# Optimization experiments

Measured on AMD Instinct MI355X. Metric: run time of the kernel, lower is better.

The kernel has to match this reference:

```python
import jax, jax.numpy as jnp
import numpy as np

NUM_EXPERTS = 8
TOP_K = 2


def setup_inputs() -> dict:
    key = jax.random.key(0)
    k1, k2, k3, k4, k5 = jax.random.split(key, 5)
    H, F, E = 1024, 4096, NUM_EXPERTS
    s = 0.02
    return {
        "hidden_states": jax.random.normal(k1, (2, 2048, H), jnp.float32),
        "w_router": jax.random.normal(k2, (E, H), jnp.float32) * s,
        "w1": jax.random.normal(k3, (E, F, H), jnp.float32) * s,
        "w2": jax.random.normal(k4, (E, H, F), jnp.float32) * s,
        "w3": jax.random.normal(k5, (E, F, H), jnp.float32) * s,
    }


def reference(hidden_states, w_router, w1, w2, w3):
    B, S, H = hidden_states.shape
    x = hidden_states.reshape(-1, H)  # [T, H]
    T = x.shape[0]
    # router (nn.Linear, no bias): logits = x @ W^T
    router_logits = x @ w_router.T  # [T, E]
    probs = jax.nn.softmax(router_logits.astype(jnp.float32), axis=-1)
    top_w, top_e = jax.lax.top_k(probs, TOP_K)  # [T, K]
    top_w = top_w / jnp.sum(top_w, axis=-1, keepdims=True)
    top_w = top_w.astype(x.dtype)
    # dense per-token gate matrix [T, E]; zero where expert not selected
    gates = jnp.zeros((T, NUM_EXPERTS), x.dtype).at[
        jnp.arange(T)[:, None], top_e
    ].add(top_w)
    out = jnp.zeros_like(x)
    for e in range(NUM_EXPERTS):  # fixed small expert loop
        h = jax.nn.silu(x @ w1[e].T) * (x @ w3[e].T)  # [T, F]
        out = out + gates[:, e:e + 1] * (h @ w2[e].T)
    return out.reshape(B, S, H), router_logits
```

## Files before the change

### kernel.cpp

```cpp
#include <hip/hip_runtime.h>
#include <hip/hip_bf16.h>
#include <stdint.h>

#define T_TOK 4096
#define H_DIM 1024
#define F_DIM 4096
#define NE 8

typedef float    f32x4  __attribute__((ext_vector_type(4)));
typedef __bf16   bf16x8 __attribute__((ext_vector_type(8)));
typedef uint16_t u16x8  __attribute__((ext_vector_type(8)));

#define AS1 __attribute__((address_space(1)))
#define AS3 __attribute__((address_space(3)))

__device__ __forceinline__ uint16_t f2bf(float f) {
  return __builtin_bit_cast(uint16_t, __float2bfloat16(f));
}

__device__ __forceinline__ void gld16(const void* g, void* l) {
  __builtin_amdgcn_global_load_lds((const AS1 void*)g, (AS3 void*)l, 16, 0, 0);
}

__global__ __launch_bounds__(256) void router_k(
    const float* __restrict__ x, const float* __restrict__ wr,
    float* __restrict__ logits, uint16_t* __restrict__ xb,
    int* __restrict__ pairTok, float* __restrict__ pairGate,
    int* __restrict__ cnt)
{
  const int lane = threadIdx.x & 63;
  const int wid  = threadIdx.x >> 6;
  const int t    = blockIdx.x * 4 + wid;

  const float* xp = x + (size_t)t * H_DIM + lane * 16;
  f32x4 xv[4];
#pragma unroll
  for (int i = 0; i < 4; ++i) xv[i] = *(const f32x4*)(xp + 4 * i);

  u16x8 o0, o1;
#pragma unroll
  for (int j = 0; j < 4; ++j) {
    o0[j] = f2bf(xv[0][j]); o0[j + 4] = f2bf(xv[1][j]);
    o1[j] = f2bf(xv[2][j]); o1[j + 4] = f2bf(xv[3][j]);
  }
  uint16_t* xbp = xb + (size_t)t * H_DIM + lane * 16;
  *(u16x8*)xbp       = o0;
  *(u16x8*)(xbp + 8) = o1;

  float s[NE];
#pragma unroll
  for (int e = 0; e < NE; ++e) {
    const float* wp = wr + e * H_DIM + lane * 16;
    float acc = 0.f;
#pragma unroll
    for (int i = 0; i < 4; ++i) {
      f32x4 wv = *(const f32x4*)(wp + 4 * i);
#pragma unroll
      for (int j = 0; j < 4; ++j) acc += xv[i][j] * wv[j];
    }
#pragma unroll
    for (int off = 32; off > 0; off >>= 1) acc += __shfl_xor(acc, off, 64);
    s[e] = acc;
  }

  if (lane == 0) {
#pragma unroll
    for (int e = 0; e < NE; ++e) logits[t * NE + e] = s[e];
    int e1 = 0;
#pragma unroll
    for (int e = 1; e < NE; ++e) if (s[e] > s[e1]) e1 = e;
    int e2 = (e1 == 0) ? 1 : 0;
#pragma unroll
    for (int e = 0; e < NE; ++e)
      if (e != e1 && e != e2 && s[e] > s[e2]) e2 = e;
    const float d  = s[e2] - s[e1];
    const float g1 = 1.f / (1.f + __expf(d));
    const float g2 = 1.f - g1;
    int i1 = atomicAdd(cnt + e1, 1);
    pairTok[e1 * T_TOK + i1] = t;  pairGate[e1 * T_TOK + i1] = g1;
    int i2 = atomicAdd(cnt + e2, 1);
    pairTok[e2 * T_TOK + i2] = t;  pairGate[e2 * T_TOK + i2] = g2;
  }
}

__global__ void prefix_k(const int* __restrict__ cnt, int* __restrict__ base) {
  if (threadIdx.x == 0) {
    int b = 0;
#pragma unroll
    for (int e = 0; e < NE; ++e) { base[e] = b; b += cnt[e]; }
  }
}

__global__ __launch_bounds__(256, 2) void ffn1_k(
    const uint16_t* __restrict__ xb, const float* __restrict__ w1,
    const float* __restrict__ w3, uint16_t* __restrict__ hbuf,
    const int* __restrict__ pairTok, const int* __restrict__ cnt,
    const int* __restrict__ base)
{
  const int e    = blockIdx.z;
  const int cnte = cnt[e];
  const int m0   = blockIdx.y * 128;
  if (m0 >= cnte) return;
  const int n0   = blockIdx.x * 128;
  const int tid  = threadIdx.x;
  const int lane = tid & 63;
  const int wid  = tid >> 6;
  const int wm   = (wid >> 1) * 64;
  const int wn   = (wid & 1) * 64;

  __shared__ __align__(16) uint16_t lsA [128 * 64];
  __shared__ __align__(16) uint16_t lsB1[128 * 64];
  __shared__ __align__(16) uint16_t lsB3[128 * 64];

  const float* w1e = w1 + (size_t)e * F_DIM * H_DIM;
  const float* w3e = w3 + (size_t)e * F_DIM * H_DIM;

  const uint16_t* asrc[4];
  const float*    b1src[4];
  const float*    b3src[4];
#pragma unroll
  for (int q = 0; q < 4; ++q) {
    const int c = q * 256 + tid;
    const int row = c >> 3, pos = c & 7;
    const int kc  = pos ^ (row & 7);
    int ar = m0 + row; if (ar >= cnte) ar = cnte - 1;
    const int tok = pairTok[e * T_TOK + ar];
    asrc[q]  = xb + (size_t)tok * H_DIM + kc * 8;
    b1src[q] = w1e + (size_t)(n0 + row) * H_DIM + kc * 8;
    b3src[q] = w3e + (size_t)(n0 + row) * H_DIM + kc * 8;
  }

  const f32x4 fz = {0.f, 0.f, 0.f, 0.f};
  f32x4 acc1[4][4], acc3[4][4];
#pragma unroll
  for (int i = 0; i < 4; ++i)
#pragma unroll
    for (int j = 0; j < 4; ++j) { acc1[i][j] = fz; acc3[i][j] = fz; }

  for (int kt = 0; kt < H_DIM; kt += 64) {
    __syncthreads();
#pragma unroll
    for (int q = 0; q < 4; ++q) {
      const int c = q * 256 + tid;
      gld16(asrc[q] + kt, &lsA[c * 8]);
    }
#pragma unroll
    for (int q = 0; q < 4; ++q) {
      const int c = q * 256 + tid;
      const float* s1 = b1src[q] + kt;
      const float* s3 = b3src[q] + kt;
      f32x4 a0 = *(const f32x4*)s1;
      f32x4 a1 = *(const f32x4*)(s1 + 4);
      f32x4 c0 = *(const f32x4*)s3;
      f32x4 c1 = *(const f32x4*)(s3 + 4);
      u16x8 ob1, ob3;
#pragma unroll
      for (int j = 0; j < 4; ++j) {
        ob1[j] = f2bf(a0[j]); ob1[j + 4] = f2bf(a1[j]);
        ob3[j] = f2bf(c0[j]); ob3[j + 4] = f2bf(c1[j]);
      }
      *(u16x8*)&lsB1[c * 8] = ob1;
      *(u16x8*)&lsB3[c * 8] = ob3;
    }
    __syncthreads();
#pragma unroll
    for (int ks = 0; ks < 2; ++ks) {
      bf16x8 af[4], b1f[4], b3f[4];
      const int kg = ks * 4 + (lane >> 4);
#pragma unroll
      for (int i = 0; i < 4; ++i) {
        const int ar = wm + i * 16 + (lane & 15);
        af[i]  = *(const bf16x8*)&lsA [ar * 64 + ((kg ^ (ar & 7)) * 8)];
        const int br = wn + i * 16 + (lane & 15);
        b1f[i] = *(const bf16x8*)&lsB1[br * 64 + ((kg ^ (br & 7)) * 8)];
        b3f[i] = *(const bf16x8*)&lsB3[br * 64 + ((kg ^ (br & 7)) * 8)];
      }
#pragma unroll
      for (int i = 0; i < 4; ++i)
#pragma unroll
        for (int j = 0; j < 4; ++j) {
          acc1[i][j] = __builtin_amdgcn_mfma_f32_16x16x32_bf16(af[i], b1f[j], acc1[i][j], 0, 0, 0);
          acc3[i][j] = __builtin_amdgcn_mfma_f32_16x16x32_bf16(af[i], b3f[j], acc3[i][j], 0, 0, 0);
        }
    }
  }

  const int be = base[e];
#pragma unroll
  for (int i = 0; i < 4; ++i) {
#pragma unroll
    for (int r = 0; r < 4; ++r) {
      const int lrow = m0 + wm + i * 16 + (lane >> 4) * 4 + r;
      if (lrow < cnte) {
        uint16_t* hp = hbuf + (size_t)(be + lrow) * F_DIM + n0 + wn + (lane & 15);
#pragma unroll
        for (int j = 0; j < 4; ++j) {
          const float a  = acc1[i][j][r];
          const float hv = (a / (1.f + __expf(-a))) * acc3[i][j][r];
          hp[j * 16] = f2bf(hv);
        }
      }
    }
  }
}

__global__ __launch_bounds__(256, 2) void ffn2_k(
    const uint16_t* __restrict__ hbuf, const float* __restrict__ w2,
    float* __restrict__ out, const int* __restrict__ pairTok,
    const float* __restrict__ pairGate, const int* __restrict__ cnt,
    const int* __restrict__ base)
{
  const int e    = blockIdx.z;
  const int cnte = cnt[e];
  const int m0   = blockIdx.y * 128;
  if (m0 >= cnte) return;
  const int n0   = blockIdx.x * 128;
  const int tid  = threadIdx.x;
  const int lane = tid & 63;
  const int wid  = tid >> 6;
  const int wm   = (wid >> 1) * 64;
  const int wn   = (wid & 1) * 64;

  __shared__ __align__(16) uint16_t lsA[128 * 64];
  __shared__ __align__(16) uint16_t lsB[128 * 64];

  const int be = base[e];
  const float* w2e = w2 + (size_t)e * H_DIM * F_DIM;

  const uint16_t* asrc[4];
  const float*    bsrc[4];
#pragma unroll
  for (int q = 0; q < 4; ++q) {
    const int c = q * 256 + tid;
    const int row = c >> 3, pos = c & 7;
    const int kc  = pos ^ (row & 7);
    int rr = m0 + row; if (rr >= cnte) rr = cnte - 1;
    asrc[q] = hbuf + (size_t)(be + rr) * F_DIM + kc * 8;
    bsrc[q] = w2e + (size_t)(n0 + row) * F_DIM + kc * 8;
  }

  const f32x4 fz = {0.f, 0.f, 0.f, 0.f};
  f32x4 acc[4][4];
#pragma unroll
  for (int i = 0; i < 4; ++i)
#pragma unroll
    for (int j = 0; j < 4; ++j) acc[i][j] = fz;

  for (int kt = 0; kt < F_DIM; kt += 64) {
    __syncthreads();
#pragma unroll
    for (int q = 0; q < 4; ++q) {
      const int c = q * 256 + tid;
      gld16(asrc[q] + kt, &lsA[c * 8]);
    }
#pragma unroll
    for (int q = 0; q < 4; ++q) {
      const int c = q * 256 + tid;
      const float* sb = bsrc[q] + kt;
      f32x4 b0 = *(const f32x4*)sb;
      f32x4 b1 = *(const f32x4*)(sb + 4);
      u16x8 ob;
#pragma unroll
      for (int j = 0; j < 4; ++j) { ob[j] = f2bf(b0[j]); ob[j + 4] = f2bf(b1[j]); }
      *(u16x8*)&lsB[c * 8] = ob;
    }
    __syncthreads();
#pragma unroll
    for (int ks = 0; ks < 2; ++ks) {
      bf16x8 af[4], bf[4];
      const int kg = ks * 4 + (lane >> 4);
#pragma unroll
      for (int i = 0; i < 4; ++i) {
        const int ar = wm + i * 16 + (lane & 15);
        af[i] = *(const bf16x8*)&lsA[ar * 64 + ((kg ^ (ar & 7)) * 8)];
        const int br = wn + i * 16 + (lane & 15);
        bf[i] = *(const bf16x8*)&lsB[br * 64 + ((kg ^ (br & 7)) * 8)];
      }
#pragma unroll
      for (int i = 0; i < 4; ++i)
#pragma unroll
        for (int j = 0; j < 4; ++j)
          acc[i][j] = __builtin_amdgcn_mfma_f32_16x16x32_bf16(af[i], bf[j], acc[i][j], 0, 0, 0);
    }
  }

#pragma unroll
  for (int i = 0; i < 4; ++i) {
#pragma unroll
    for (int r = 0; r < 4; ++r) {
      const int lrow = m0 + wm + i * 16 + (lane >> 4) * 4 + r;
      if (lrow < cnte) {
        const int   t = pairTok [e * T_TOK + lrow];
        const float g = pairGate[e * T_TOK + lrow];
        float* op = out + (size_t)t * H_DIM + n0 + wn + (lane & 15);
#pragma unroll
        for (int j = 0; j < 4; ++j)
          unsafeAtomicAdd(op + j * 16, g * acc[i][j][r]);
      }
    }
  }
}

extern "C" void kernel_launch(void* const* d_in, const int* in_sizes, int n_in,
                              void* d_out, int out_size, void* d_ws, size_t ws_size,
                              hipStream_t stream)
{
  const float* x  = (const float*)d_in[0];
  const float* wr = (const float*)d_in[1];
  const float* w1 = (const float*)d_in[2];
  const float* w2 = (const float*)d_in[3];
  const float* w3 = (const float*)d_in[4];
  float* out    = (float*)d_out;
  float* logits = out + (size_t)T_TOK * H_DIM;

  uint8_t* ws = (uint8_t*)d_ws;
  const size_t XB_OFF   = 0;
  const size_t HB_OFF   = XB_OFF + (size_t)T_TOK * H_DIM * 2;
  const size_t PT_OFF   = HB_OFF + (size_t)2 * T_TOK * F_DIM * 2;
  const size_t PG_OFF   = PT_OFF + (size_t)NE * T_TOK * 4;
  const size_t CNT_OFF  = PG_OFF + (size_t)NE * T_TOK * 4;
  const size_t BASE_OFF = CNT_OFF + 64;
  const size_t NEED     = BASE_OFF + 64;
  if (ws_size < NEED) return;

  uint16_t* xb      = (uint16_t*)(ws + XB_OFF);
  uint16_t* hb      = (uint16_t*)(ws + HB_OFF);
  int*      pairTok = (int*)(ws + PT_OFF);
  float*    pairGate= (float*)(ws + PG_OFF);
  int*      cnt     = (int*)(ws + CNT_OFF);
  int*      basep   = (int*)(ws + BASE_OFF);

  hipMemsetAsync(out, 0, (size_t)T_TOK * H_DIM * sizeof(float), stream);
  hipMemsetAsync(cnt, 0, 64, stream);
  router_k<<<T_TOK / 4, 256, 0, stream>>>(x, wr, logits, xb, pairTok, pairGate, cnt);
  prefix_k<<<1, 64, 0, stream>>>(cnt, basep);
  ffn1_k<<<dim3(F_DIM / 128, T_TOK / 128, NE), 256, 0, stream>>>(xb, w1, w3, hb, pairTok, cnt, basep);
  ffn2_k<<<dim3(H_DIM / 128, T_TOK / 128, NE), 256, 0, stream>>>(hb, w2, out, pairTok, pairGate, cnt, basep);
}
```

Measured before the change: 569.9 us.

## Pre-convert expert weights to bf16 and stream them via direct LDS loads

Adds a conversion kernel that turns w1, w3 and w2 into bf16 copies in workspace on every call. New FFN kernels then load both activations and weights with global_load_lds into XOR-swizzled LDS tiles, replacing the fp32 weight loads with in-kernel conversion. The extra pass reads about 400MB of fp32 weights and writes 200MB of bf16, in exchange for simpler, cheaper GEMM inner loops. This path runs only if the workspace holds the three bf16 weight copies; otherwise the old kernels are used.

Result: slower. 742.4 us (+30.3%).

```diff
diff --git a/kernel.cpp b/kernel.cpp
--- a/kernel.cpp
+++ b/kernel.cpp
@@ -20,6 +20,20 @@
 
 __device__ __forceinline__ void gld16(const void* g, void* l) {
   __builtin_amdgcn_global_load_lds((const AS1 void*)g, (AS3 void*)l, 16, 0, 0);
+}
+
+__global__ __launch_bounds__(256) void cvt_k(const float* __restrict__ src,
+                                             uint16_t* __restrict__ dst, int n8) {
+  const int stride = gridDim.x * blockDim.x;
+  for (int i = blockIdx.x * blockDim.x + threadIdx.x; i < n8; i += stride) {
+    const float* s = src + (size_t)i * 8;
+    f32x4 a = *(const f32x4*)s;
+    f32x4 b = *(const f32x4*)(s + 4);
+    u16x8 o;
+#pragma unroll
+    for (int j = 0; j < 4; ++j) { o[j] = f2bf(a[j]); o[j + 4] = f2bf(b[j]); }
+    *(u16x8*)(dst + (size_t)i * 8) = o;
+  }
 }
 
 __global__ __launch_bounds__(256) void router_k(
@@ -90,6 +104,192 @@
     for (int e = 0; e < NE; ++e) { base[e] = b; b += cnt[e]; }
   }
 }
+
+
+__global__ __launch_bounds__(256, 3) void ffn1b_k(
+    const uint16_t* __restrict__ xb, const uint16_t* __restrict__ w1b,
+    const uint16_t* __restrict__ w3b, uint16_t* __restrict__ hbuf,
+    const int* __restrict__ pairTok, const int* __restrict__ cnt,
+    const int* __restrict__ base)
+{
+  const int e    = blockIdx.z;
+  const int cnte = cnt[e];
+  const int m0   = blockIdx.y * 128;
+  if (m0 >= cnte) return;
+  const int n0   = blockIdx.x * 128;
+  const int tid  = threadIdx.x;
+  const int lane = tid & 63;
+  const int wid  = tid >> 6;
+  const int wm   = (wid >> 1) * 64;
+  const int wn   = (wid & 1) * 64;
+
+  __shared__ __align__(16) uint16_t lsA [128 * 64];
+  __shared__ __align__(16) uint16_t lsB1[128 * 64];
+  __shared__ __align__(16) uint16_t lsB3[128 * 64];
+
+  const uint16_t* w1e = w1b + (size_t)e * F_DIM * H_DIM;
+  const uint16_t* w3e = w3b + (size_t)e * F_DIM * H_DIM;
+
+  const uint16_t* asrc[4];
+  const uint16_t* b1src[4];
+  const uint16_t* b3src[4];
+#pragma unroll
+  for (int q = 0; q < 4; ++q) {
+    const int c = q * 256 + tid;
+    const int row = c >> 3, pos = c & 7;
+    const int kc  = pos ^ (row & 7);
+    int ar = m0 + row; if (ar >= cnte) ar = cnte - 1;
+    const int tok = pairTok[e * T_TOK + ar];
+    asrc[q]  = xb  + (size_t)tok * H_DIM + kc * 8;
+    b1src[q] = w1e + (size_t)(n0 + row) * H_DIM + kc * 8;
+    b3src[q] = w3e + (size_t)(n0 + row) * H_DIM + kc * 8;
+  }
+
+  const f32x4 fz = {0.f, 0.f, 0.f, 0.f};
+  f32x4 acc1[4][4], acc3[4][4];
+#pragma unroll
+  for (int i = 0; i < 4; ++i)
+#pragma unroll
+    for (int j = 0; j < 4; ++j) { acc1[i][j] = fz; acc3[i][j] = fz; }
+
+  for (int kt = 0; kt < H_DIM; kt += 64) {
+    __syncthreads();
+#pragma unroll
+    for (int q = 0; q < 4; ++q) {
+      const int c = q * 256 + tid;
+      gld16(asrc[q]  + kt, &lsA [c * 8]);
+      gld16(b1src[q] + kt, &lsB1[c * 8]);
+      gld16(b3src[q] + kt, &lsB3[c * 8]);
+    }
+    __syncthreads();
+#pragma unroll
+    for (int ks = 0; ks < 2; ++ks) {
+      bf16x8 af[4], b1f[4], b3f[4];
+      const int kg = ks * 4 + (lane >> 4);
+#pragma unroll
+      for (int i = 0; i < 4; ++i) {
+        const int ar = wm + i * 16 + (lane & 15);
+        af[i]  = *(const bf16x8*)&lsA [ar * 64 + ((kg ^ (ar & 7)) * 8)];
+        const int br = wn + i * 16 + (lane & 15);
+        b1f[i] = *(const bf16x8*)&lsB1[br * 64 + ((kg ^ (br & 7)) * 8)];
+        b3f[i] = *(const bf16x8*)&lsB3[br * 64 + ((kg ^ (br & 7)) * 8)];
+      }
+#pragma unroll
+      for (int i = 0; i < 4; ++i)
+#pragma unroll
+        for (int j = 0; j < 4; ++j) {
+          acc1[i][j] = __builtin_amdgcn_mfma_f32_16x16x32_bf16(af[i], b1f[j], acc1[i][j], 0, 0, 0);
+          acc3[i][j] = __builtin_amdgcn_mfma_f32_16x16x32_bf16(af[i], b3f[j], acc3[i][j], 0, 0, 0);
+        }
+    }
+  }
+
+  const int be = base[e];
+#pragma unroll
+  for (int i = 0; i < 4; ++i) {
+#pragma unroll
+    for (int r = 0; r < 4; ++r) {
+      const int lrow = m0 + wm + i * 16 + (lane >> 4) * 4 + r;
+      if (lrow < cnte) {
+        uint16_t* hp = hbuf + (size_t)(be + lrow) * F_DIM + n0 + wn + (lane & 15);
+#pragma unroll
+        for (int j = 0; j < 4; ++j) {
+          const float a  = acc1[i][j][r];
+          const float hv = (a / (1.f + __expf(-a))) * acc3[i][j][r];
+          hp[j * 16] = f2bf(hv);
+        }
+      }
+    }
+  }
+}
+
+__global__ __launch_bounds__(256, 3) void ffn2b_k(
+    const uint16_t* __restrict__ hbuf, const uint16_t* __restrict__ w2b,
+    float* __restrict__ out, const int* __restrict__ pairTok,
+    const float* __restrict__ pairGate, const int* __restrict__ cnt,
+    const int* __restrict__ base)
+{
+  const int e    = blockIdx.z;
+  const int cnte = cnt[e];
+  const int m0   = blockIdx.y * 128;
+  if (m0 >= cnte) return;
+  const int n0   = blockIdx.x * 128;
+  const int tid  = threadIdx.x;
+  const int lane = tid & 63;
+  const int wid  = tid >> 6;
+  const int wm   = (wid >> 1) * 64;
+  const int wn   = (wid & 1) * 64;
+
+  __shared__ __align__(16) uint16_t lsA[128 * 64];
+  __shared__ __align__(16) uint16_t lsB[128 * 64];
+
+  const int be = base[e];
+  const uint16_t* w2e = w2b + (size_t)e * H_DIM * F_DIM;
+
+  const uint16_t* asrc[4];
+  const uint16_t* bsrc[4];
+#pragma unroll
+  for (int q = 0; q < 4; ++q) {
+    const int c = q * 256 + tid;
+    const int row = c >> 3, pos = c & 7;
+    const int kc  = pos ^ (row & 7);
+    int rr = m0 + row; if (rr >= cnte) rr = cnte - 1;
+    asrc[q] = hbuf + (size_t)(be + rr) * F_DIM + kc * 8;
+    bsrc[q] = w2e + (size_t)(n0 + row) * F_DIM + kc * 8;
+  }
+
+  const f32x4 fz = {0.f, 0.f, 0.f, 0.f};
+  f32x4 acc[4][4];
+#pragma unroll
+  for (int i = 0; i < 4; ++i)
+#pragma unroll
+    for (int j = 0; j < 4; ++j) acc[i][j] = fz;
+
+  for (int kt = 0; kt < F_DIM; kt += 64) {
+    __syncthreads();
+#pragma unroll
+    for (int q = 0; q < 4; ++q) {
+      const int c = q * 256 + tid;
+      gld16(asrc[q] + kt, &lsA[c * 8]);
+      gld16(bsrc[q] + kt, &lsB[c * 8]);
+    }
+    __syncthreads();
+#pragma unroll
+    for (int ks = 0; ks < 2; ++ks) {
+      bf16x8 af[4], bf[4];
+      const int kg = ks * 4 + (lane >> 4);
+#pragma unroll
+      for (int i = 0; i < 4; ++i) {
+        const int ar = wm + i * 16 + (lane & 15);
+        af[i] = *(const bf16x8*)&lsA[ar * 64 + ((kg ^ (ar & 7)) * 8)];
+        const int br = wn + i * 16 + (lane & 15);
+        bf[i] = *(const bf16x8*)&lsB[br * 64 + ((kg ^ (br & 7)) * 8)];
+      }
+#pragma unroll
+      for (int i = 0; i < 4; ++i)
+#pragma unroll
+        for (int j = 0; j < 4; ++j)
+          acc[i][j] = __builtin_amdgcn_mfma_f32_16x16x32_bf16(af[i], bf[j], acc[i][j], 0, 0, 0);
+    }
+  }
+
+#pragma unroll
+  for (int i = 0; i < 4; ++i) {
+#pragma unroll
+    for (int r = 0; r < 4; ++r) {
+      const int lrow = m0 + wm + i * 16 + (lane >> 4) * 4 + r;
+      if (lrow < cnte) {
+        const int   t = pairTok [e * T_TOK + lrow];
+        const float g = pairGate[e * T_TOK + lrow];
+        float* op = out + (size_t)t * H_DIM + n0 + wn + (lane & 15);
+#pragma unroll
+        for (int j = 0; j < 4; ++j)
+          unsafeAtomicAdd(op + j * 16, g * acc[i][j][r]);
+      }
+    }
+  }
+}
+
 
 __global__ __launch_bounds__(256, 2) void ffn1_k(
     const uint16_t* __restrict__ xb, const float* __restrict__ w1,
@@ -314,14 +514,19 @@
   float* logits = out + (size_t)T_TOK * H_DIM;
 
   uint8_t* ws = (uint8_t*)d_ws;
+  const size_t WELEMS   = (size_t)NE * F_DIM * H_DIM;
   const size_t XB_OFF   = 0;
   const size_t HB_OFF   = XB_OFF + (size_t)T_TOK * H_DIM * 2;
   const size_t PT_OFF   = HB_OFF + (size_t)2 * T_TOK * F_DIM * 2;
   const size_t PG_OFF   = PT_OFF + (size_t)NE * T_TOK * 4;
   const size_t CNT_OFF  = PG_OFF + (size_t)NE * T_TOK * 4;
   const size_t BASE_OFF = CNT_OFF + 64;
-  const size_t NEED     = BASE_OFF + 64;
-  if (ws_size < NEED) return;
+  const size_t W1B_OFF  = BASE_OFF + 64;
+  const size_t W3B_OFF  = W1B_OFF + WELEMS * 2;
+  const size_t W2B_OFF  = W3B_OFF + WELEMS * 2;
+  const size_t NEED_BIG = W2B_OFF + WELEMS * 2;
+  const size_t NEED_SM  = W1B_OFF;
+  if (ws_size < NEED_SM) return;
 
   uint16_t* xb      = (uint16_t*)(ws + XB_OFF);
   uint16_t* hb      = (uint16_t*)(ws + HB_OFF);
@@ -334,6 +539,19 @@
   hipMemsetAsync(cnt, 0, 64, stream);
   router_k<<<T_TOK / 4, 256, 0, stream>>>(x, wr, logits, xb, pairTok, pairGate, cnt);
   prefix_k<<<1, 64, 0, stream>>>(cnt, basep);
-  ffn1_k<<<dim3(F_DIM / 128, T_TOK / 128, NE), 256, 0, stream>>>(xb, w1, w3, hb, pairTok, cnt, basep);
-  ffn2_k<<<dim3(H_DIM / 128, T_TOK / 128, NE), 256, 0, stream>>>(hb, w2, out, pairTok, pairGate, cnt, basep);
-}
+
+  if (ws_size >= NEED_BIG) {
+    uint16_t* w1b = (uint16_t*)(ws + W1B_OFF);
+    uint16_t* w3b = (uint16_t*)(ws + W3B_OFF);
+    uint16_t* w2b = (uint16_t*)(ws + W2B_OFF);
+    const int n8 = (int)(WELEMS / 8);
+    cvt_k<<<2048, 256, 0, stream>>>(w1, w1b, n8);
+    cvt_k<<<2048, 256, 0, stream>>>(w3, w3b, n8);
+    cvt_k<<<2048, 256, 0, stream>>>(w2, w2b, n8);
+    ffn1b_k<<<dim3(F_DIM / 128, T_TOK / 128, NE), 256, 0, stream>>>(xb, w1b, w3b, hb, pairTok, cnt, basep);
+    ffn2b_k<<<dim3(H_DIM / 128, T_TOK / 128, NE), 256, 0, stream>>>(hb, w2b, out, pairTok, pairGate, cnt, basep);
+  } else {
+    ffn1_k<<<dim3(F_DIM / 128, T_TOK / 128, NE), 256, 0, stream>>>(xb, w1, w3, hb, pairTok, cnt, basep);
+    ffn2_k<<<dim3(H_DIM / 128, T_TOK / 128, NE), 256, 0, stream>>>(hb, w2, out, pairTok, pairGate, cnt, basep);
+  }
+}
```

## Double-buffer LDS tiles with register prefetch in both FFN GEMM kernels

Applied to the files above, without the earlier changes.

Both expert GEMM kernels now use two LDS stages with a K-tile of 32 instead of one stage of 64. The next tile's global loads (direct-to-LDS for activations, register loads for fp32 weights) are issued before the MFMA work on the current tile, and the converted weights are stored afterwards, so only one barrier is needed per iteration. This is meant to hide global-load latency behind compute. The trade-off is twice as many loop iterations with shallower MFMA work per barrier, plus extra registers for the prefetched values; ffn2 also raises its launch-bounds occupancy hint from 2 to 3.

Result: slower. 685.5 us (+20.3%).

```diff
diff --git a/kernel.cpp b/kernel.cpp
--- a/kernel.cpp
+++ b/kernel.cpp
@@ -108,24 +108,26 @@
   const int wm   = (wid >> 1) * 64;
   const int wn   = (wid & 1) * 64;
 
-  __shared__ __align__(16) uint16_t lsA [128 * 64];
-  __shared__ __align__(16) uint16_t lsB1[128 * 64];
-  __shared__ __align__(16) uint16_t lsB3[128 * 64];
+  __shared__ __align__(16) uint16_t lsA [2][128 * 32];
+  __shared__ __align__(16) uint16_t lsB1[2][128 * 32];
+  __shared__ __align__(16) uint16_t lsB3[2][128 * 32];
 
   const float* w1e = w1 + (size_t)e * F_DIM * H_DIM;
   const float* w3e = w3 + (size_t)e * F_DIM * H_DIM;
 
-  const uint16_t* asrc[4];
-  const float*    b1src[4];
-  const float*    b3src[4];
-#pragma unroll
-  for (int q = 0; q < 4; ++q) {
+  const uint16_t* asrc[2];
+  const float*    b1src[2];
+  const float*    b3src[2];
+  int cdst[2];
+#pragma unroll
+  for (int q = 0; q < 2; ++q) {
     const int c = q * 256 + tid;
-    const int row = c >> 3, pos = c & 7;
-    const int kc  = pos ^ (row & 7);
+    const int row = c >> 2, pos = c & 3;
+    const int kc  = pos ^ (row & 3);
+    cdst[q] = c * 8;
     int ar = m0 + row; if (ar >= cnte) ar = cnte - 1;
     const int tok = pairTok[e * T_TOK + ar];
-    asrc[q]  = xb + (size_t)tok * H_DIM + kc * 8;
+    asrc[q]  = xb  + (size_t)tok * H_DIM + kc * 8;
     b1src[q] = w1e + (size_t)(n0 + row) * H_DIM + kc * 8;
     b3src[q] = w3e + (size_t)(n0 + row) * H_DIM + kc * 8;
   }
@@ -137,43 +139,57 @@
 #pragma unroll
     for (int j = 0; j < 4; ++j) { acc1[i][j] = fz; acc3[i][j] = fz; }
 
-  for (int kt = 0; kt < H_DIM; kt += 64) {
-    __syncthreads();
-#pragma unroll
-    for (int q = 0; q < 4; ++q) {
-      const int c = q * 256 + tid;
-      gld16(asrc[q] + kt, &lsA[c * 8]);
-    }
-#pragma unroll
-    for (int q = 0; q < 4; ++q) {
-      const int c = q * 256 + tid;
-      const float* s1 = b1src[q] + kt;
-      const float* s3 = b3src[q] + kt;
-      f32x4 a0 = *(const f32x4*)s1;
-      f32x4 a1 = *(const f32x4*)(s1 + 4);
-      f32x4 c0 = *(const f32x4*)s3;
-      f32x4 c1 = *(const f32x4*)(s3 + 4);
+  {
+#pragma unroll
+    for (int q = 0; q < 2; ++q) gld16(asrc[q], &lsA[0][cdst[q]]);
+#pragma unroll
+    for (int q = 0; q < 2; ++q) {
+      f32x4 a0 = *(const f32x4*)b1src[q];
+      f32x4 a1 = *(const f32x4*)(b1src[q] + 4);
+      f32x4 c0 = *(const f32x4*)b3src[q];
+      f32x4 c1 = *(const f32x4*)(b3src[q] + 4);
       u16x8 ob1, ob3;
 #pragma unroll
       for (int j = 0; j < 4; ++j) {
         ob1[j] = f2bf(a0[j]); ob1[j + 4] = f2bf(a1[j]);
         ob3[j] = f2bf(c0[j]); ob3[j + 4] = f2bf(c1[j]);
       }
-      *(u16x8*)&lsB1[c * 8] = ob1;
-      *(u16x8*)&lsB3[c * 8] = ob3;
-    }
-    __syncthreads();
-#pragma unroll
-    for (int ks = 0; ks < 2; ++ks) {
+      *(u16x8*)&lsB1[0][cdst[q]] = ob1;
+      *(u16x8*)&lsB3[0][cdst[q]] = ob3;
+    }
+  }
+  __syncthreads();
+
+  const int NT = H_DIM / 32;
+  for (int t = 0; t < NT; ++t) {
+    const int cur = t & 1;
+    const int nxt = cur ^ 1;
+    const int koff = (t + 1) * 32;
+    const bool pre = (t + 1 < NT);
+
+    f32x4 b1v[2][2], b3v[2][2];
+    if (pre) {
+#pragma unroll
+      for (int q = 0; q < 2; ++q) gld16(asrc[q] + koff, &lsA[nxt][cdst[q]]);
+#pragma unroll
+      for (int q = 0; q < 2; ++q) {
+        b1v[q][0] = *(const f32x4*)(b1src[q] + koff);
+        b1v[q][1] = *(const f32x4*)(b1src[q] + koff + 4);
+        b3v[q][0] = *(const f32x4*)(b3src[q] + koff);
+        b3v[q][1] = *(const f32x4*)(b3src[q] + koff + 4);
+      }
+    }
+
+    {
       bf16x8 af[4], b1f[4], b3f[4];
-      const int kg = ks * 4 + (lane >> 4);
+      const int kg = lane >> 4;
 #pragma unroll
       for (int i = 0; i < 4; ++i) {
         const int ar = wm + i * 16 + (lane & 15);
-        af[i]  = *(const bf16x8*)&lsA [ar * 64 + ((kg ^ (ar & 7)) * 8)];
+        af[i]  = *(const bf16x8*)&lsA [cur][ar * 32 + ((kg ^ (ar & 3)) * 8)];
         const int br = wn + i * 16 + (lane & 15);
-        b1f[i] = *(const bf16x8*)&lsB1[br * 64 + ((kg ^ (br & 7)) * 8)];
-        b3f[i] = *(const bf16x8*)&lsB3[br * 64 + ((kg ^ (br & 7)) * 8)];
+        b1f[i] = *(const bf16x8*)&lsB1[cur][br * 32 + ((kg ^ (br & 3)) * 8)];
+        b3f[i] = *(const bf16x8*)&lsB3[cur][br * 32 + ((kg ^ (br & 3)) * 8)];
       }
 #pragma unroll
       for (int i = 0; i < 4; ++i)
@@ -183,6 +199,21 @@
           acc3[i][j] = __builtin_amdgcn_mfma_f32_16x16x32_bf16(af[i], b3f[j], acc3[i][j], 0, 0, 0);
         }
     }
+
+    if (pre) {
+#pragma unroll
+      for (int q = 0; q < 2; ++q) {
+        u16x8 ob1, ob3;
+#pragma unroll
+        for (int j = 0; j < 4; ++j) {
+          ob1[j] = f2bf(b1v[q][0][j]); ob1[j + 4] = f2bf(b1v[q][1][j]);
+          ob3[j] = f2bf(b3v[q][0][j]); ob3[j + 4] = f2bf(b3v[q][1][j]);
+        }
+        *(u16x8*)&lsB1[nxt][cdst[q]] = ob1;
+        *(u16x8*)&lsB3[nxt][cdst[q]] = ob3;
+      }
+    }
+    __syncthreads();
   }
 
   const int be = base[e];
@@ -204,7 +235,7 @@
   }
 }
 
-__global__ __launch_bounds__(256, 2) void ffn2_k(
+__global__ __launch_bounds__(256, 3) void ffn2_k(
     const uint16_t* __restrict__ hbuf, const float* __restrict__ w2,
     float* __restrict__ out, const int* __restrict__ pairTok,
     const float* __restrict__ pairGate, const int* __restrict__ cnt,
@@ -221,19 +252,21 @@
   const int wm   = (wid >> 1) * 64;
   const int wn   = (wid & 1) * 64;
 
-  __shared__ __align__(16) uint16_t lsA[128 * 64];
-  __shared__ __align__(16) uint16_t lsB[128 * 64];
+  __shared__ __align__(16) uint16_t lsA[2][128 * 32];
+  __shared__ __align__(16) uint16_t lsB[2][128 * 32];
 
   const int be = base[e];
   const float* w2e = w2 + (size_t)e * H_DIM * F_DIM;
 
-  const uint16_t* asrc[4];
-  const float*    bsrc[4];
-#pragma unroll
-  for (int q = 0; q < 4; ++q) {
+  const uint16_t* asrc[2];
+  const float*    bsrc[2];
+  int cdst[2];
+#pragma unroll
+  for (int q = 0; q < 2; ++q) {
     const int c = q * 256 + tid;
-    const int row = c >> 3, pos = c & 7;
-    const int kc  = pos ^ (row & 7);
+    const int row = c >> 2, pos = c & 3;
+    const int kc  = pos ^ (row & 3);
+    cdst[q] = c * 8;
     int rr = m0 + row; if (rr >= cnte) rr = cnte - 1;
     asrc[q] = hbuf + (size_t)(be + rr) * F_DIM + kc * 8;
     bsrc[q] = w2e + (size_t)(n0 + row) * F_DIM + kc * 8;
@@ -246,35 +279,48 @@
 #pragma unroll
     for (int j = 0; j < 4; ++j) acc[i][j] = fz;
 
-  for (int kt = 0; kt < F_DIM; kt += 64) {
-    __syncthreads();
-#pragma unroll
-    for (int q = 0; q < 4; ++q) {
-      const int c = q * 256 + tid;
-      gld16(asrc[q] + kt, &lsA[c * 8]);
-    }
-#pragma unroll
-    for (int q = 0; q < 4; ++q) {
-      const int c = q * 256 + tid;
-      const float* sb = bsrc[q] + kt;
-      f32x4 b0 = *(const f32x4*)sb;
-      f32x4 b1 = *(const f32x4*)(sb + 4);
+  {
+#pragma unroll
+    for (int q = 0; q < 2; ++q) gld16(asrc[q], &lsA[0][cdst[q]]);
+#pragma unroll
+    for (int q = 0; q < 2; ++q) {
+      f32x4 b0 = *(const f32x4*)bsrc[q];
+      f32x4 b1 = *(const f32x4*)(bsrc[q] + 4);
       u16x8 ob;
 #pragma unroll
       for (int j = 0; j < 4; ++j) { ob[j] = f2bf(b0[j]); ob[j + 4] = f2bf(b1[j]); }
-      *(u16x8*)&lsB[c * 8] = ob;
-    }
-    __syncthreads();
-#pragma unroll
-    for (int ks = 0; ks < 2; ++ks) {
+      *(u16x8*)&lsB[0][cdst[q]] = ob;
+    }
+  }
+  __syncthreads();
+
+  const int NT = F_DIM / 32;
+  for (int t = 0; t < NT; ++t) {
+    const int cur = t & 1;
+    const int nxt = cur ^ 1;
+    const int koff = (t + 1) * 32;
+    const bool pre = (t + 1 < NT);
+
+    f32x4 bv[2][2];
+    if (pre) {
+#pragma unroll
+      for (int q = 0; q < 2; ++q) gld16(asrc[q] + koff, &lsA[nxt][cdst[q]]);
+#pragma unroll
+      for (int q = 0; q < 2; ++q) {
+        bv[q][0] = *(const f32x4*)(bsrc[q] + koff);
+        bv[q][1] = *(const f32x4*)(bsrc[q] + koff + 4);
+      }
+    }
+
+    {
       bf16x8 af[4], bf[4];
-      const int kg = ks * 4 + (lane >> 4);
+      const int kg = lane >> 4;
 #pragma unroll
       for (int i = 0; i < 4; ++i) {
         const int ar = wm + i * 16 + (lane & 15);
-        af[i] = *(const bf16x8*)&lsA[ar * 64 + ((kg ^ (ar & 7)) * 8)];
+        af[i] = *(const bf16x8*)&lsA[cur][ar * 32 + ((kg ^ (ar & 3)) * 8)];
         const int br = wn + i * 16 + (lane & 15);
-        bf[i] = *(const bf16x8*)&lsB[br * 64 + ((kg ^ (br & 7)) * 8)];
+        bf[i] = *(const bf16x8*)&lsB[cur][br * 32 + ((kg ^ (br & 3)) * 8)];
       }
 #pragma unroll
       for (int i = 0; i < 4; ++i)
@@ -282,6 +328,17 @@
         for (int j = 0; j < 4; ++j)
           acc[i][j] = __builtin_amdgcn_mfma_f32_16x16x32_bf16(af[i], bf[j], acc[i][j], 0, 0, 0);
     }
+
+    if (pre) {
+#pragma unroll
+      for (int q = 0; q < 2; ++q) {
+        u16x8 ob;
+#pragma unroll
+        for (int j = 0; j < 4; ++j) { ob[j] = f2bf(bv[q][0][j]); ob[j + 4] = f2bf(bv[q][1][j]); }
+        *(u16x8*)&lsB[nxt][cdst[q]] = ob;
+      }
+    }
+    __syncthreads();
   }
 
 #pragma unroll
```

## Replace LDS-tiled ffn1 with register-direct MFMA loads and double buffering

Applied to the files above, without the earlier changes.

Rewrites the gate/up projection kernel to skip shared memory and barriers, loading A and B fragments straight from global memory into registers. Tiles become 256 tokens by 32 columns, and loads are software-pipelined with two register sets. This removes LDS traffic and sync overhead. In exchange, the gathered activation rows are re-read far more often across the many narrow column blocks, and weight reads are less coalesced.

Result: slower. 1.081 ms (+89.8%).

```diff
diff --git a/kernel.cpp b/kernel.cpp
--- a/kernel.cpp
+++ b/kernel.cpp
@@ -99,106 +99,91 @@
 {
   const int e    = blockIdx.z;
   const int cnte = cnt[e];
-  const int m0   = blockIdx.y * 128;
+  const int m0   = blockIdx.y * 256;
   if (m0 >= cnte) return;
-  const int n0   = blockIdx.x * 128;
-  const int tid  = threadIdx.x;
-  const int lane = tid & 63;
-  const int wid  = tid >> 6;
-  const int wm   = (wid >> 1) * 64;
-  const int wn   = (wid & 1) * 64;
-
-  __shared__ __align__(16) uint16_t lsA [128 * 64];
-  __shared__ __align__(16) uint16_t lsB1[128 * 64];
-  __shared__ __align__(16) uint16_t lsB3[128 * 64];
-
-  const float* w1e = w1 + (size_t)e * F_DIM * H_DIM;
-  const float* w3e = w3 + (size_t)e * F_DIM * H_DIM;
-
-  const uint16_t* asrc[4];
-  const float*    b1src[4];
-  const float*    b3src[4];
-#pragma unroll
-  for (int q = 0; q < 4; ++q) {
-    const int c = q * 256 + tid;
-    const int row = c >> 3, pos = c & 7;
-    const int kc  = pos ^ (row & 7);
-    int ar = m0 + row; if (ar >= cnte) ar = cnte - 1;
+  const int n0   = blockIdx.x * 32;
+  const int lane = threadIdx.x & 63;
+  const int wid  = threadIdx.x >> 6;
+  const int wm   = (wid >> 1) * 128;
+  const int wn   = (wid & 1) * 16;
+  const int kg8  = (lane >> 4) * 8;
+
+  const uint16_t* aptr[8];
+#pragma unroll
+  for (int i = 0; i < 8; ++i) {
+    int ar = m0 + wm + i * 16 + (lane & 15);
+    if (ar >= cnte) ar = cnte - 1;
     const int tok = pairTok[e * T_TOK + ar];
-    asrc[q]  = xb + (size_t)tok * H_DIM + kc * 8;
-    b1src[q] = w1e + (size_t)(n0 + row) * H_DIM + kc * 8;
-    b3src[q] = w3e + (size_t)(n0 + row) * H_DIM + kc * 8;
-  }
+    aptr[i] = xb + (size_t)tok * H_DIM + kg8;
+  }
+  const int   nrow = n0 + wn + (lane & 15);
+  const float* b1p = w1 + (size_t)e * F_DIM * H_DIM + (size_t)nrow * H_DIM + kg8;
+  const float* b3p = w3 + (size_t)e * F_DIM * H_DIM + (size_t)nrow * H_DIM + kg8;
 
   const f32x4 fz = {0.f, 0.f, 0.f, 0.f};
-  f32x4 acc1[4][4], acc3[4][4];
-#pragma unroll
-  for (int i = 0; i < 4; ++i)
-#pragma unroll
-    for (int j = 0; j < 4; ++j) { acc1[i][j] = fz; acc3[i][j] = fz; }
-
-  for (int kt = 0; kt < H_DIM; kt += 64) {
-    __syncthreads();
-#pragma unroll
-    for (int q = 0; q < 4; ++q) {
-      const int c = q * 256 + tid;
-      gld16(asrc[q] + kt, &lsA[c * 8]);
-    }
-#pragma unroll
-    for (int q = 0; q < 4; ++q) {
-      const int c = q * 256 + tid;
-      const float* s1 = b1src[q] + kt;
-      const float* s3 = b3src[q] + kt;
-      f32x4 a0 = *(const f32x4*)s1;
-      f32x4 a1 = *(const f32x4*)(s1 + 4);
-      f32x4 c0 = *(const f32x4*)s3;
-      f32x4 c1 = *(const f32x4*)(s3 + 4);
-      u16x8 ob1, ob3;
-#pragma unroll
-      for (int j = 0; j < 4; ++j) {
-        ob1[j] = f2bf(a0[j]); ob1[j + 4] = f2bf(a1[j]);
-        ob3[j] = f2bf(c0[j]); ob3[j + 4] = f2bf(c1[j]);
-      }
-      *(u16x8*)&lsB1[c * 8] = ob1;
-      *(u16x8*)&lsB3[c * 8] = ob3;
-    }
-    __syncthreads();
-#pragma unroll
-    for (int ks = 0; ks < 2; ++ks) {
-      bf16x8 af[4], b1f[4], b3f[4];
-      const int kg = ks * 4 + (lane >> 4);
-#pragma unroll
-      for (int i = 0; i < 4; ++i) {
-        const int ar = wm + i * 16 + (lane & 15);
-        af[i]  = *(const bf16x8*)&lsA [ar * 64 + ((kg ^ (ar & 7)) * 8)];
-        const int br = wn + i * 16 + (lane & 15);
-        b1f[i] = *(const bf16x8*)&lsB1[br * 64 + ((kg ^ (br & 7)) * 8)];
-        b3f[i] = *(const bf16x8*)&lsB3[br * 64 + ((kg ^ (br & 7)) * 8)];
-      }
-#pragma unroll
-      for (int i = 0; i < 4; ++i)
-#pragma unroll
-        for (int j = 0; j < 4; ++j) {
-          acc1[i][j] = __builtin_amdgcn_mfma_f32_16x16x32_bf16(af[i], b1f[j], acc1[i][j], 0, 0, 0);
-          acc3[i][j] = __builtin_amdgcn_mfma_f32_16x16x32_bf16(af[i], b3f[j], acc3[i][j], 0, 0, 0);
-        }
-    }
-  }
-
-  const int be = base[e];
-#pragma unroll
-  for (int i = 0; i < 4; ++i) {
+  f32x4 acc1[8], acc3[8];
+#pragma unroll
+  for (int i = 0; i < 8; ++i) { acc1[i] = fz; acc3[i] = fz; }
+
+#define LOAD_A(dst, kk)                                                   \
+  _Pragma("unroll") for (int i = 0; i < 8; ++i)                           \
+      dst[i] = *(const bf16x8*)(aptr[i] + (kk) * 32);
+
+#define LOAD_B(d1, d3, kk)                                                \
+  d1##0 = *(const f32x4*)(b1p + (kk) * 32);                               \
+  d1##1 = *(const f32x4*)(b1p + (kk) * 32 + 4);                           \
+  d3##0 = *(const f32x4*)(b3p + (kk) * 32);                               \
+  d3##1 = *(const f32x4*)(b3p + (kk) * 32 + 4);
+
+#define TILE(aset, r1, r3)                                                \
+  {                                                                       \
+    u16x8 u1, u3;                                                         \
+    _Pragma("unroll") for (int j = 0; j < 4; ++j) {                       \
+      u1[j] = f2bf(r1##0[j]); u1[j + 4] = f2bf(r1##1[j]);                 \
+      u3[j] = f2bf(r3##0[j]); u3[j + 4] = f2bf(r3##1[j]);                 \
+    }                                                                     \
+    const bf16x8 b1f = __builtin_bit_cast(bf16x8, u1);                    \
+    const bf16x8 b3f = __builtin_bit_cast(bf16x8, u3);                    \
+    _Pragma("unroll") for (int i = 0; i < 8; ++i) {                       \
+      acc1[i] = __builtin_amdgcn_mfma_f32_16x16x32_bf16(aset[i], b1f, acc1[i], 0, 0, 0); \
+      acc3[i] = __builtin_amdgcn_mfma_f32_16x16x32_bf16(aset[i], b3f, acc3[i], 0, 0, 0); \
+    }                                                                     \
+  }
+
+  bf16x8 aA[8], aB[8];
+  f32x4 r1A0, r1A1, r3A0, r3A1;
+  f32x4 r1B0, r1B1, r3B0, r3B1;
+
+  LOAD_A(aA, 0)
+  LOAD_B(r1A, r3A, 0)
+
+#pragma unroll
+  for (int tt = 0; tt < 16; ++tt) {
+    const int t = tt * 2;
+    LOAD_A(aB, t + 1)
+    LOAD_B(r1B, r3B, t + 1)
+    TILE(aA, r1A, r3A)
+    if (t + 2 < 32) {
+      LOAD_A(aA, t + 2)
+      LOAD_B(r1A, r3A, t + 2)
+    }
+    TILE(aB, r1B, r3B)
+  }
+#undef LOAD_A
+#undef LOAD_B
+#undef TILE
+
+  const int be  = base[e];
+  const int col = n0 + wn + (lane & 15);
+#pragma unroll
+  for (int i = 0; i < 8; ++i) {
 #pragma unroll
     for (int r = 0; r < 4; ++r) {
       const int lrow = m0 + wm + i * 16 + (lane >> 4) * 4 + r;
       if (lrow < cnte) {
-        uint16_t* hp = hbuf + (size_t)(be + lrow) * F_DIM + n0 + wn + (lane & 15);
-#pragma unroll
-        for (int j = 0; j < 4; ++j) {
-          const float a  = acc1[i][j][r];
-          const float hv = (a / (1.f + __expf(-a))) * acc3[i][j][r];
-          hp[j * 16] = f2bf(hv);
-        }
+        const float a  = acc1[i][r];
+        const float hv = (a / (1.f + __expf(-a))) * acc3[i][r];
+        hbuf[(size_t)(be + lrow) * F_DIM + col] = f2bf(hv);
       }
     }
   }
@@ -334,6 +319,6 @@
   hipMemsetAsync(cnt, 0, 64, stream);
   router_k<<<T_TOK / 4, 256, 0, stream>>>(x, wr, logits, xb, pairTok, pairGate, cnt);
   prefix_k<<<1, 64, 0, stream>>>(cnt, basep);
-  ffn1_k<<<dim3(F_DIM / 128, T_TOK / 128, NE), 256, 0, stream>>>(xb, w1, w3, hb, pairTok, cnt, basep);
+  ffn1_k<<<dim3(F_DIM / 32, T_TOK / 256, NE), 256, 0, stream>>>(xb, w1, w3, hb, pairTok, cnt, basep);
   ffn2_k<<<dim3(H_DIM / 128, T_TOK / 128, NE), 256, 0, stream>>>(hb, w2, out, pairTok, pairGate, cnt, basep);
 }
```
